# Kernel optimization log

Hardware: AMD Instinct MI355X
Metric: run time of the kernel (lower is better)

The kernel has to match this reference:

```python
import jax, jax.numpy as jnp
import numpy as np
import math

N_NODES = 100000
N_EDGES = 3200000
F_IN = 512
HID = 128
N_CLS = 16


def setup_inputs() -> dict:
    key = jax.random.key(0)
    k = jax.random.split(key, 6)
    x = jax.random.normal(k[0], (N_NODES, F_IN), dtype=jnp.float32)
    edge_index = jax.random.randint(k[1], (2, N_EDGES), 0, N_NODES, dtype=jnp.int32)
    W1 = jax.random.normal(k[2], (F_IN, HID), dtype=jnp.float32) / np.sqrt(F_IN)
    W2 = jax.random.normal(k[3], (HID, HID), dtype=jnp.float32) / np.sqrt(HID)
    W3 = jax.random.normal(k[4], (N_CLS, HID), dtype=jnp.float32) / np.sqrt(HID)
    b3 = jnp.zeros((N_CLS,), dtype=jnp.float32)
    return {"x": x, "edge_index": edge_index, "W1": W1, "W2": W2, "W3": W3, "b3": b3}


def _sym_norm(edge_index, num_nodes, dtype):
    # add self loops with fill_value = trunc(log2(average_node_degree))
    E = edge_index.shape[1]
    fill = float(math.trunc(math.log2(E / num_nodes)))
    loops = jnp.arange(num_nodes, dtype=edge_index.dtype)
    row = jnp.concatenate([edge_index[0], loops])
    col = jnp.concatenate([edge_index[1], loops])
    w = jnp.concatenate([jnp.ones((E,), dtype), jnp.full((num_nodes,), fill, dtype)])
    deg = jax.ops.segment_sum(w, row, num_segments=num_nodes)
    deg_inv_sqrt = jnp.where(deg > 0, jax.lax.rsqrt(deg), 0.0)
    norm = deg_inv_sqrt[row] * w * deg_inv_sqrt[col]
    return row, col, norm


def reference(x, edge_index, W1, W2, W3, b3):
    N = x.shape[0]
    row, col, norm = _sym_norm(edge_index, N, x.dtype)

    def gcn(h, W):
        h = h @ W                                   # [N, d_out]
        msg = norm[:, None] * h[col]                # gather + scale, [E', d_out]
        return jax.ops.segment_sum(msg, row, num_segments=N)

    h = jax.nn.relu(gcn(x, W1))      # layer 1 + srelu (threshold clamped at 0)
    h = gcn(h, W2)                   # layer 2
    # dropout p=0.5 is identity in eval mode
    return h @ W3.T + b3             # linear classifier [N, n_classes]
```

## Files before the change

kernel.cpp:

```cpp
#include <hip/hip_runtime.h>
#include <cmath>

typedef __attribute__((ext_vector_type(8))) short short8;
typedef __attribute__((ext_vector_type(8))) unsigned short ushort8;
typedef __attribute__((ext_vector_type(4))) float f32x4;
typedef __attribute__((ext_vector_type(2))) float f32x2;
typedef __attribute__((ext_vector_type(4))) unsigned int uint4v;
typedef __attribute__((ext_vector_type(2))) int int2v;

#define EPB 4096
#define BCAP 20480

__device__ inline float bf16_lo(unsigned int p) {
  union { unsigned int i; float f; } v; v.i = p << 16; return v.f;
}
__device__ inline float bf16_hi(unsigned int p) {
  union { unsigned int i; float f; } v; v.i = p & 0xffff0000u; return v.f;
}
__device__ inline f32x2 bf2(unsigned int p) {
  union { unsigned int i; float f; } lo, hi;
  lo.i = p << 16;
  hi.i = p & 0xffff0000u;
  return (f32x2){lo.f, hi.f};
}
__device__ inline float bf16u(unsigned short w) {
  union { unsigned int i; float f; } v; v.i = (unsigned int)w << 16; return v.f;
}
__device__ inline unsigned short f32_to_bf16(float f) {
  union { float f; unsigned int i; } v; v.f = f;
  unsigned int x = v.i;
  x += 0x7fffu + ((x >> 16) & 1u);
  return (unsigned short)(x >> 16);
}
__device__ inline unsigned int cvt_pk_bf16(float a, float b) {
  unsigned int r;
  asm("v_cvt_pk_bf16_f32 %0, %1, %2" : "=v"(r) : "v"(a), "v"(b));
  return r;
}
__device__ inline f32x2 pk_add(f32x2 a, f32x2 b) {
  f32x2 d;
  asm("v_pk_add_f32 %0, %1, %2" : "=v"(d) : "v"(a), "v"(b));
  return d;
}

__global__ __launch_bounds__(256) void bin_k(const int* __restrict__ rows,
                                             const int* __restrict__ cols,
                                             int* __restrict__ bucket_cursor,
                                             unsigned int* __restrict__ binned, int E) {
  __shared__ int lhist[256];
  __shared__ int gbase[256];
  __shared__ int loff[256];
  const int t = threadIdx.x;
  const int base = blockIdx.x * EPB;
  lhist[t] = 0;
  __syncthreads();

  int bk[16];
  unsigned int pk[16];
#pragma unroll
  for (int j = 0; j < 16; ++j) {
    int e = base + j * 256 + t;
    if (e < E) {
      int r = rows[e];
      int c = cols[e];
      bk[j] = r >> 9;
      pk[j] = ((unsigned int)(r & 511) << 17) | (unsigned int)c;
      atomicAdd(&lhist[bk[j]], 1);
    } else {
      bk[j] = -1;
    }
  }
  __syncthreads();
  if (lhist[t] > 0) gbase[t] = atomicAdd(&bucket_cursor[t], lhist[t]);
  loff[t] = 0;
  __syncthreads();
#pragma unroll
  for (int j = 0; j < 16; ++j) {
    if (bk[j] >= 0) {
      int rank = gbase[bk[j]] + atomicAdd(&loff[bk[j]], 1);
      if (rank < BCAP) binned[(size_t)bk[j] * BCAP + rank] = pk[j];
    }
  }
}

__global__ __launch_bounds__(1024) void bucket_csr_k(const unsigned int* __restrict__ binned,
                                                     const int* __restrict__ bucket_cursor,
                                                     int2v* __restrict__ rowse,
                                                     float* __restrict__ dis,
                                                     int* __restrict__ col_sorted,
                                                     int* __restrict__ perm,
                                                     int N, float fill) {
  __shared__ int lcnt[512];
  __shared__ int dh[512];
  __shared__ int wsum[16];
  const int b = blockIdx.x;
  const int t = threadIdx.x;
  const int start = b * BCAP;
  int cnt = bucket_cursor[b];
  if (cnt > BCAP) cnt = BCAP;
  const int endb = start + cnt;
  const int rbase = b << 9;

  auto scan512 = [&](int v) -> int {
    int x = v;
#pragma unroll
    for (int d = 1; d < 64; d <<= 1) {
      int u = __shfl_up(x, d, 64);
      if ((t & 63) >= d) x += u;
    }
    if (t < 512 && (t & 63) == 63) wsum[t >> 6] = x;
    __syncthreads();
    if (t < 64) {
      int s = (t < 8) ? wsum[t] : 0;
#pragma unroll
      for (int d = 1; d < 8; d <<= 1) {
        int u = __shfl_up(s, d, 64);
        if (t >= d) s += u;
      }
      if (t < 8) wsum[t] = s;
    }
    __syncthreads();
    int off = (t >= 64 && t < 512) ? wsum[(t >> 6) - 1] : 0;
    return x + off;
  };

  if (t < 512) lcnt[t] = 0;
  __syncthreads();
  for (int i = start + t; i < endb; i += 1024)
    atomicAdd(&lcnt[binned[i] >> 17], 1);
  __syncthreads();

  int v = (t < 512) ? lcnt[t] : 0;
  int incl = scan512(v);
  if (t < 512) {
    int excl = incl - v;
    int r = rbase + t;
    if (r < N) {
      rowse[r] = (int2v){start + excl, start + excl + v};
      float d = (float)v + fill;
      dis[r] = d > 0.f ? rsqrtf(d) : 0.f;
    }
    lcnt[t] = excl;
  }
  __syncthreads();

  if (t < 512) dh[t] = 0;
  __syncthreads();
  int key = 0;
  if (t < 512) {
    key = 511 - (v < 511 ? v : 511);
    atomicAdd(&dh[key], 1);
  }
  __syncthreads();
  int hv = (t < 512) ? dh[t] : 0;
  int hincl = scan512(hv);
  if (t < 512) dh[t] = hincl - hv;
  __syncthreads();
  if (t < 512) {
    int rank = atomicAdd(&dh[key], 1);
    perm[(b << 9) + rank] = rbase + t;
  }
  __syncthreads();

  for (int i = start + t; i < endb; i += 1024) {
    unsigned int pk = binned[i];
    int rl = (int)(pk >> 17);
    int c = (int)(pk & 0x1FFFFu);
    int pos = atomicAdd(&lcnt[rl], 1);
    col_sorted[start + pos] = c;
  }
}

__global__ __launch_bounds__(256) void cast_w_k(const float* __restrict__ W1,
                                                const float* __restrict__ W2,
                                                const float* __restrict__ W3,
                                                unsigned short* __restrict__ W1t,
                                                unsigned short* __restrict__ W2t,
                                                unsigned short* __restrict__ W3b,
                                                int FIN) {
  int g = blockIdx.x * 256 + threadIdx.x;
  int n1 = FIN * 128;
  if (g < n1) {
    int n = g & 127, k = g >> 7;
    W1t[n * FIN + k] = f32_to_bf16(W1[(size_t)k * 128 + n]);
  } else if (g < n1 + 128 * 128) {
    int gg = g - n1;
    int n = gg & 127, k = gg >> 7;
    W2t[n * 128 + k] = f32_to_bf16(W2[k * 128 + n]);
  } else if (g < n1 + 128 * 128 + 16 * 128) {
    int gg = g - n1 - 128 * 128;
    W3b[gg] = f32_to_bf16(W3[gg]);
  }
}

__global__ __launch_bounds__(256) void gemm_k(const void* __restrict__ Aq, int a_is_f32,
                                              int M, int K,
                                              const unsigned short* __restrict__ Bt,
                                              const float* __restrict__ dis,
                                              unsigned short* __restrict__ C) {
  __shared__ unsigned short Al[128 * 40];
  __shared__ unsigned short Bl[128 * 40];
  const int t = threadIdx.x;
  const int bm = blockIdx.x * 128;
  const int lane = t & 63;
  const int wave = t >> 6;
  const int wm = (wave >> 1) * 64;
  const int wn = (wave & 1) * 64;
  const int l15 = lane & 15;
  const int l4 = lane >> 4;

  f32x4 acc[4][4];
#pragma unroll
  for (int a = 0; a < 4; ++a)
#pragma unroll
    for (int b = 0; b < 4; ++b) acc[a][b] = (f32x4){0.f, 0.f, 0.f, 0.f};

  const int am = t >> 1;
  const int ak = (t & 1) * 16;
  const int bn = t >> 1;
  const int bk = (t & 1) * 16;
  const int arow = bm + am;
  const bool arow_ok = arow < M;

  auto load_a = [&](int k0, ushort8& o0, ushort8& o1) {
    o0 = (ushort8){0, 0, 0, 0, 0, 0, 0, 0};
    o1 = (ushort8){0, 0, 0, 0, 0, 0, 0, 0};
    if (arow_ok) {
      if (a_is_f32) {
        const float* p = (const float*)Aq + (size_t)arow * K + k0 + ak;
        f32x4 f0 = *(const f32x4*)(p);
        f32x4 f1 = *(const f32x4*)(p + 4);
        f32x4 f2 = *(const f32x4*)(p + 8);
        f32x4 f3 = *(const f32x4*)(p + 12);
        union { unsigned int u[4]; ushort8 v8; } c0, c1;
        c0.u[0] = cvt_pk_bf16(f0[0], f0[1]);
        c0.u[1] = cvt_pk_bf16(f0[2], f0[3]);
        c0.u[2] = cvt_pk_bf16(f1[0], f1[1]);
        c0.u[3] = cvt_pk_bf16(f1[2], f1[3]);
        c1.u[0] = cvt_pk_bf16(f2[0], f2[1]);
        c1.u[1] = cvt_pk_bf16(f2[2], f2[3]);
        c1.u[2] = cvt_pk_bf16(f3[0], f3[1]);
        c1.u[3] = cvt_pk_bf16(f3[2], f3[3]);
        o0 = c0.v8;
        o1 = c1.v8;
      } else {
        const unsigned short* p = (const unsigned short*)Aq + (size_t)arow * K + k0 + ak;
        o0 = *(const ushort8*)p;
        o1 = *(const ushort8*)(p + 8);
      }
    }
  };

  ushort8 av0, av1;
  load_a(0, av0, av1);
  ushort8 bv0 = *(const ushort8*)(Bt + (size_t)bn * K + bk);
  ushort8 bv1 = *(const ushort8*)(Bt + (size_t)bn * K + bk + 8);

  for (int k0 = 0; k0 < K; k0 += 32) {
    *(ushort8*)&Al[am * 40 + ak] = av0;
    *(ushort8*)&Al[am * 40 + ak + 8] = av1;
    *(ushort8*)&Bl[bn * 40 + bk] = bv0;
    *(ushort8*)&Bl[bn * 40 + bk + 8] = bv1;
    __syncthreads();

    const int kn = k0 + 32;
    if (kn < K) {
      load_a(kn, av0, av1);
      bv0 = *(const ushort8*)(Bt + (size_t)bn * K + kn + bk);
      bv1 = *(const ushort8*)(Bt + (size_t)bn * K + kn + bk + 8);
    }

    short8 af[4];
#pragma unroll
    for (int mt = 0; mt < 4; ++mt)
      af[mt] = *(const short8*)&Al[(wm + mt * 16 + l15) * 40 + l4 * 8];
#pragma unroll
    for (int nt = 0; nt < 4; ++nt) {
      short8 bfr = *(const short8*)&Bl[(wn + nt * 16 + l15) * 40 + l4 * 8];
#pragma unroll
      for (int mt = 0; mt < 4; ++mt)
        acc[mt][nt] = __builtin_amdgcn_mfma_f32_16x16x32_bf16(af[mt], bfr, acc[mt][nt], 0, 0, 0);
    }
    __syncthreads();
  }

#pragma unroll
  for (int mt = 0; mt < 4; ++mt) {
    int rbase = bm + wm + mt * 16 + l4 * 4;
#pragma unroll
    for (int r = 0; r < 4; ++r) {
      int row = rbase + r;
      if (row < M) {
        float dr = dis[row];
#pragma unroll
        for (int nt = 0; nt < 4; ++nt) {
          int col = wn + nt * 16 + l15;
          C[(size_t)row * 128 + col] = f32_to_bf16(acc[mt][nt][r] * dr);
        }
      }
    }
  }
}

__global__ __launch_bounds__(256) void agg_k(const unsigned short* __restrict__ hs,
                                             const int2v* __restrict__ rowse,
                                             const int* __restrict__ cols,
                                             const float* __restrict__ dis,
                                             const int* __restrict__ perm,
                                             unsigned short* __restrict__ out_bf,
                                             const unsigned short* __restrict__ W3b,
                                             const float* __restrict__ b3,
                                             float* __restrict__ fcout,
                                             int N, float fill, int mode) {
  const int q = blockIdx.x * 16 + (threadIdx.x >> 4);
  const unsigned int fl = threadIdx.x & 15;
  const int rid = __builtin_nontemporal_load(&perm[q]);
  if (rid >= N) return;
  const char* __restrict__ hsc = (const char*)hs;
  const unsigned int flo = fl << 4;

  int2v se = __builtin_nontemporal_load(&rowse[rid]);
  int e = se.x;
  const int end = se.y;

  f32x2 a0 = {0.f, 0.f}, a1 = {0.f, 0.f}, a2 = {0.f, 0.f}, a3 = {0.f, 0.f};

  for (; e + 8 <= end; e += 8) {
    unsigned int c0 = (unsigned int)__builtin_nontemporal_load(&cols[e]);
    unsigned int c1 = (unsigned int)__builtin_nontemporal_load(&cols[e + 1]);
    unsigned int c2 = (unsigned int)__builtin_nontemporal_load(&cols[e + 2]);
    unsigned int c3 = (unsigned int)__builtin_nontemporal_load(&cols[e + 3]);
    unsigned int c4 = (unsigned int)__builtin_nontemporal_load(&cols[e + 4]);
    unsigned int c5 = (unsigned int)__builtin_nontemporal_load(&cols[e + 5]);
    unsigned int c6 = (unsigned int)__builtin_nontemporal_load(&cols[e + 6]);
    unsigned int c7 = (unsigned int)__builtin_nontemporal_load(&cols[e + 7]);
    uint4v p0 = *(const uint4v*)(hsc + ((c0 << 8) | flo));
    uint4v p1 = *(const uint4v*)(hsc + ((c1 << 8) | flo));
    uint4v p2 = *(const uint4v*)(hsc + ((c2 << 8) | flo));
    uint4v p3 = *(const uint4v*)(hsc + ((c3 << 8) | flo));
    uint4v p4 = *(const uint4v*)(hsc + ((c4 << 8) | flo));
    uint4v p5 = *(const uint4v*)(hsc + ((c5 << 8) | flo));
    uint4v p6 = *(const uint4v*)(hsc + ((c6 << 8) | flo));
    uint4v p7 = *(const uint4v*)(hsc + ((c7 << 8) | flo));
    a0 = pk_add(a0, bf2(p0[0])); a1 = pk_add(a1, bf2(p0[1]));
    a2 = pk_add(a2, bf2(p0[2])); a3 = pk_add(a3, bf2(p0[3]));
    a0 = pk_add(a0, bf2(p1[0])); a1 = pk_add(a1, bf2(p1[1]));
    a2 = pk_add(a2, bf2(p1[2])); a3 = pk_add(a3, bf2(p1[3]));
    a0 = pk_add(a0, bf2(p2[0])); a1 = pk_add(a1, bf2(p2[1]));
    a2 = pk_add(a2, bf2(p2[2])); a3 = pk_add(a3, bf2(p2[3]));
    a0 = pk_add(a0, bf2(p3[0])); a1 = pk_add(a1, bf2(p3[1]));
    a2 = pk_add(a2, bf2(p3[2])); a3 = pk_add(a3, bf2(p3[3]));
    a0 = pk_add(a0, bf2(p4[0])); a1 = pk_add(a1, bf2(p4[1]));
    a2 = pk_add(a2, bf2(p4[2])); a3 = pk_add(a3, bf2(p4[3]));
    a0 = pk_add(a0, bf2(p5[0])); a1 = pk_add(a1, bf2(p5[1]));
    a2 = pk_add(a2, bf2(p5[2])); a3 = pk_add(a3, bf2(p5[3]));
    a0 = pk_add(a0, bf2(p6[0])); a1 = pk_add(a1, bf2(p6[1]));
    a2 = pk_add(a2, bf2(p6[2])); a3 = pk_add(a3, bf2(p6[3]));
    a0 = pk_add(a0, bf2(p7[0])); a1 = pk_add(a1, bf2(p7[1]));
    a2 = pk_add(a2, bf2(p7[2])); a3 = pk_add(a3, bf2(p7[3]));
  }
  for (; e + 4 <= end; e += 4) {
    unsigned int c0 = (unsigned int)__builtin_nontemporal_load(&cols[e]);
    unsigned int c1 = (unsigned int)__builtin_nontemporal_load(&cols[e + 1]);
    unsigned int c2 = (unsigned int)__builtin_nontemporal_load(&cols[e + 2]);
    unsigned int c3 = (unsigned int)__builtin_nontemporal_load(&cols[e + 3]);
    uint4v p0 = *(const uint4v*)(hsc + ((c0 << 8) | flo));
    uint4v p1 = *(const uint4v*)(hsc + ((c1 << 8) | flo));
    uint4v p2 = *(const uint4v*)(hsc + ((c2 << 8) | flo));
    uint4v p3 = *(const uint4v*)(hsc + ((c3 << 8) | flo));
    a0 = pk_add(a0, bf2(p0[0])); a1 = pk_add(a1, bf2(p0[1]));
    a2 = pk_add(a2, bf2(p0[2])); a3 = pk_add(a3, bf2(p0[3]));
    a0 = pk_add(a0, bf2(p1[0])); a1 = pk_add(a1, bf2(p1[1]));
    a2 = pk_add(a2, bf2(p1[2])); a3 = pk_add(a3, bf2(p1[3]));
    a0 = pk_add(a0, bf2(p2[0])); a1 = pk_add(a1, bf2(p2[1]));
    a2 = pk_add(a2, bf2(p2[2])); a3 = pk_add(a3, bf2(p2[3]));
    a0 = pk_add(a0, bf2(p3[0])); a1 = pk_add(a1, bf2(p3[1]));
    a2 = pk_add(a2, bf2(p3[2])); a3 = pk_add(a3, bf2(p3[3]));
  }
  for (; e < end; ++e) {
    unsigned int c = (unsigned int)__builtin_nontemporal_load(&cols[e]);
    uint4v p = *(const uint4v*)(hsc + ((c << 8) | flo));
    a0 = pk_add(a0, bf2(p[0])); a1 = pk_add(a1, bf2(p[1]));
    a2 = pk_add(a2, bf2(p[2])); a3 = pk_add(a3, bf2(p[3]));
  }

  uint4v ps = *(const uint4v*)(hsc + (((unsigned int)rid << 8) | flo));
  float dr = dis[rid];
  float v[8];
  v[0] = dr * (a0.x + fill * bf16_lo(ps[0]));
  v[1] = dr * (a0.y + fill * bf16_hi(ps[0]));
  v[2] = dr * (a1.x + fill * bf16_lo(ps[1]));
  v[3] = dr * (a1.y + fill * bf16_hi(ps[1]));
  v[4] = dr * (a2.x + fill * bf16_lo(ps[2]));
  v[5] = dr * (a2.y + fill * bf16_hi(ps[2]));
  v[6] = dr * (a3.x + fill * bf16_lo(ps[3]));
  v[7] = dr * (a3.y + fill * bf16_hi(ps[3]));

  if (mode == 0) {
    uint4v o;
#pragma unroll
    for (int k = 0; k < 4; ++k) {
      float f0 = fmaxf(v[2 * k], 0.f);
      float f1 = fmaxf(v[2 * k + 1], 0.f);
      o[k] = cvt_pk_bf16(f0, f1);
    }
    __builtin_nontemporal_store(o, (uint4v*)((char*)out_bf + (((unsigned int)rid << 8) | flo)));
  } else {
    float p[16];
#pragma unroll
    for (int c = 0; c < 16; ++c) {
      ushort8 wr = *(const ushort8*)(W3b + c * 128 + fl * 8);
      float s = v[0] * bf16u(wr[0]);
      s = fmaf(v[1], bf16u(wr[1]), s);
      s = fmaf(v[2], bf16u(wr[2]), s);
      s = fmaf(v[3], bf16u(wr[3]), s);
      s = fmaf(v[4], bf16u(wr[4]), s);
      s = fmaf(v[5], bf16u(wr[5]), s);
      s = fmaf(v[6], bf16u(wr[6]), s);
      s = fmaf(v[7], bf16u(wr[7]), s);
      p[c] = s;
    }
#pragma unroll
    for (int m = 1; m <= 8; m <<= 1)
#pragma unroll
      for (int c = 0; c < 16; ++c) p[c] += __shfl_xor(p[c], m);
    fcout[(size_t)rid * 16 + fl] = p[fl] + b3[fl];
  }
}

extern "C" void kernel_launch(void* const* d_in, const int* in_sizes, int n_in,
                              void* d_out, int out_size, void* d_ws, size_t ws_size,
                              hipStream_t stream) {
  const float* x  = (const float*)d_in[0];
  const int* edge = (const int*)d_in[1];
  const float* W1 = (const float*)d_in[2];
  const float* W2 = (const float*)d_in[3];
  const float* W3 = (const float*)d_in[4];
  const float* b3 = (const float*)d_in[5];
  float* out = (float*)d_out;

  const int HID = 128;
  const int FIN = in_sizes[2] / HID;
  const int N   = in_sizes[0] / FIN;
  const int E   = in_sizes[1] / 2;
  const float fill = truncf(log2f((float)E / (float)N));

  char* w = (char*)d_ws;
  size_t off = 0;
  auto alloc = [&](size_t bytes) -> void* {
    void* p = w + off;
    off += (bytes + 255) & ~(size_t)255;
    return p;
  };
  const int NB = (N + 511) >> 9;
  float* dis      = (float*)alloc((size_t)N * 4);
  int2v* rowse    = (int2v*)alloc((size_t)N * 8);
  int* perm       = (int*)alloc((size_t)NB * 512 * 4);
  int* col_sorted = (int*)alloc((size_t)NB * BCAP * 4);
  int* bucket_cursor = (int*)alloc(256 * 4);
  unsigned int* binned = (unsigned int*)alloc((size_t)NB * BCAP * 4);
  unsigned short* W1t  = (unsigned short*)alloc((size_t)FIN * 128 * 2);
  unsigned short* W2t  = (unsigned short*)alloc(128 * 128 * 2);
  unsigned short* W3b  = (unsigned short*)alloc(16 * 128 * 2);
  unsigned short* bufA = (unsigned short*)alloc((size_t)N * 128 * 2);
  unsigned short* bufB = (unsigned short*)alloc((size_t)N * 128 * 2);

  const int* rows  = edge;
  const int* colsp = edge + E;

  hipMemsetAsync(bucket_cursor, 0, 256 * 4, stream);
  bin_k<<<(E + EPB - 1) / EPB, 256, 0, stream>>>(rows, colsp, bucket_cursor, binned, E);
  bucket_csr_k<<<NB, 1024, 0, stream>>>(binned, bucket_cursor, rowse, dis,
                                        col_sorted, perm, N, fill);
  const int castN = FIN * 128 + 128 * 128 + 16 * 128;
  cast_w_k<<<(castN + 255) / 256, 256, 0, stream>>>(W1, W2, W3, W1t, W2t, W3b, FIN);

  const int gm = (N + 127) / 128;
  gemm_k<<<gm, 256, 0, stream>>>(x, 1, N, FIN, W1t, dis, bufA);
  agg_k<<<NB * 32, 256, 0, stream>>>(bufA, rowse, col_sorted, dis, perm, bufB,
                                     W3b, b3, out, N, fill, 0);
  gemm_k<<<gm, 256, 0, stream>>>(bufB, 0, N, HID, W2t, dis, bufA);
  agg_k<<<NB * 32, 256, 0, stream>>>(bufA, rowse, col_sorted, dis, perm, bufB,
                                     W3b, b3, out, N, fill, 1);
}
```

Baseline: 670.7 us.

## Replace bucket binning CSR build with global degree count, scan, and atomic scatter

Replaces the two-pass bucket binning (shared-memory histogram, then per-bucket local sort) with a global per-row atomic degree count, a per-block scan that sets row offsets and cursors, and a global atomic scatter of columns into CSR slots. This drops the intermediate binned buffer and its read/write traffic, but adds 3.2M global atomics on row counters twice, and column order within a row becomes nondeterministic. The aggregation kernel also switches its nontemporal loads and stores to ordinary cached ones.

Result: slower. 983.8 us (+46.7%).

```diff
diff --git a/kernel.cpp b/kernel.cpp
--- a/kernel.cpp
+++ b/kernel.cpp
@@ -7,8 +7,8 @@
 typedef __attribute__((ext_vector_type(2))) float f32x2;
 typedef __attribute__((ext_vector_type(4))) unsigned int uint4v;
 typedef __attribute__((ext_vector_type(2))) int int2v;
-
-#define EPB 4096
+typedef __attribute__((ext_vector_type(4))) int int4v;
+
 #define BCAP 20480
 
 __device__ inline float bf16_lo(unsigned int p) {
@@ -43,131 +43,115 @@
   return d;
 }
 
-__global__ __launch_bounds__(256) void bin_k(const int* __restrict__ rows,
-                                             const int* __restrict__ cols,
-                                             int* __restrict__ bucket_cursor,
-                                             unsigned int* __restrict__ binned, int E) {
-  __shared__ int lhist[256];
-  __shared__ int gbase[256];
-  __shared__ int loff[256];
-  const int t = threadIdx.x;
-  const int base = blockIdx.x * EPB;
-  lhist[t] = 0;
-  __syncthreads();
-
-  int bk[16];
-  unsigned int pk[16];
-#pragma unroll
-  for (int j = 0; j < 16; ++j) {
-    int e = base + j * 256 + t;
-    if (e < E) {
-      int r = rows[e];
-      int c = cols[e];
-      bk[j] = r >> 9;
-      pk[j] = ((unsigned int)(r & 511) << 17) | (unsigned int)c;
-      atomicAdd(&lhist[bk[j]], 1);
-    } else {
-      bk[j] = -1;
-    }
-  }
-  __syncthreads();
-  if (lhist[t] > 0) gbase[t] = atomicAdd(&bucket_cursor[t], lhist[t]);
-  loff[t] = 0;
-  __syncthreads();
-#pragma unroll
-  for (int j = 0; j < 16; ++j) {
-    if (bk[j] >= 0) {
-      int rank = gbase[bk[j]] + atomicAdd(&loff[bk[j]], 1);
-      if (rank < BCAP) binned[(size_t)bk[j] * BCAP + rank] = pk[j];
-    }
-  }
-}
-
-__global__ __launch_bounds__(1024) void bucket_csr_k(const unsigned int* __restrict__ binned,
-                                                     const int* __restrict__ bucket_cursor,
-                                                     int2v* __restrict__ rowse,
-                                                     float* __restrict__ dis,
-                                                     int* __restrict__ col_sorted,
-                                                     int* __restrict__ perm,
-                                                     int N, float fill) {
-  __shared__ int lcnt[512];
+__global__ __launch_bounds__(256) void deg_k(const int* __restrict__ rows,
+                                             int* __restrict__ deg, int E) {
+  int i = (blockIdx.x * 256 + threadIdx.x) * 4;
+  if (i + 4 <= E) {
+    int4v r4 = *(const int4v*)(rows + i);
+    atomicAdd(&deg[r4[0]], 1);
+    atomicAdd(&deg[r4[1]], 1);
+    atomicAdd(&deg[r4[2]], 1);
+    atomicAdd(&deg[r4[3]], 1);
+  } else {
+    for (int e = i; e < E; ++e) atomicAdd(&deg[rows[e]], 1);
+  }
+}
+
+__global__ __launch_bounds__(512) void scan_k(const int* __restrict__ deg,
+                                              int2v* __restrict__ rowse,
+                                              float* __restrict__ dis,
+                                              int* __restrict__ cursor,
+                                              int* __restrict__ perm,
+                                              int N, float fill) {
+  __shared__ int wsum[8];
   __shared__ int dh[512];
-  __shared__ int wsum[16];
   const int b = blockIdx.x;
   const int t = threadIdx.x;
+  const int rbase = b << 9;
   const int start = b * BCAP;
-  int cnt = bucket_cursor[b];
-  if (cnt > BCAP) cnt = BCAP;
-  const int endb = start + cnt;
-  const int rbase = b << 9;
-
-  auto scan512 = [&](int v) -> int {
-    int x = v;
-#pragma unroll
-    for (int d = 1; d < 64; d <<= 1) {
-      int u = __shfl_up(x, d, 64);
-      if ((t & 63) >= d) x += u;
-    }
-    if (t < 512 && (t & 63) == 63) wsum[t >> 6] = x;
-    __syncthreads();
-    if (t < 64) {
-      int s = (t < 8) ? wsum[t] : 0;
-#pragma unroll
-      for (int d = 1; d < 8; d <<= 1) {
-        int u = __shfl_up(s, d, 64);
-        if (t >= d) s += u;
-      }
-      if (t < 8) wsum[t] = s;
-    }
-    __syncthreads();
-    int off = (t >= 64 && t < 512) ? wsum[(t >> 6) - 1] : 0;
-    return x + off;
-  };
-
-  if (t < 512) lcnt[t] = 0;
-  __syncthreads();
-  for (int i = start + t; i < endb; i += 1024)
-    atomicAdd(&lcnt[binned[i] >> 17], 1);
-  __syncthreads();
-
-  int v = (t < 512) ? lcnt[t] : 0;
-  int incl = scan512(v);
-  if (t < 512) {
-    int excl = incl - v;
-    int r = rbase + t;
-    if (r < N) {
-      rowse[r] = (int2v){start + excl, start + excl + v};
-      float d = (float)v + fill;
-      dis[r] = d > 0.f ? rsqrtf(d) : 0.f;
-    }
-    lcnt[t] = excl;
-  }
-  __syncthreads();
-
-  if (t < 512) dh[t] = 0;
-  __syncthreads();
-  int key = 0;
-  if (t < 512) {
-    key = 511 - (v < 511 ? v : 511);
-    atomicAdd(&dh[key], 1);
-  }
-  __syncthreads();
-  int hv = (t < 512) ? dh[t] : 0;
-  int hincl = scan512(hv);
-  if (t < 512) dh[t] = hincl - hv;
-  __syncthreads();
-  if (t < 512) {
-    int rank = atomicAdd(&dh[key], 1);
-    perm[(b << 9) + rank] = rbase + t;
-  }
-  __syncthreads();
-
-  for (int i = start + t; i < endb; i += 1024) {
-    unsigned int pk = binned[i];
-    int rl = (int)(pk >> 17);
-    int c = (int)(pk & 0x1FFFFu);
-    int pos = atomicAdd(&lcnt[rl], 1);
-    col_sorted[start + pos] = c;
+
+  int v = deg[rbase + t];
+
+  int x = v;
+#pragma unroll
+  for (int d = 1; d < 64; d <<= 1) {
+    int u = __shfl_up(x, d, 64);
+    if ((t & 63) >= d) x += u;
+  }
+  if ((t & 63) == 63) wsum[t >> 6] = x;
+  __syncthreads();
+  if (t < 64) {
+    int s = (t < 8) ? wsum[t] : 0;
+#pragma unroll
+    for (int d = 1; d < 8; d <<= 1) {
+      int u = __shfl_up(s, d, 64);
+      if (t >= d) s += u;
+    }
+    if (t < 8) wsum[t] = s;
+  }
+  __syncthreads();
+  int incl = x + ((t >= 64) ? wsum[(t >> 6) - 1] : 0);
+  int excl = incl - v;
+
+  const int r = rbase + t;
+  if (r < N) {
+    rowse[r] = (int2v){start + excl, start + excl + v};
+    float d = (float)v + fill;
+    dis[r] = d > 0.f ? rsqrtf(d) : 0.f;
+  }
+  cursor[r] = start + excl;
+
+  dh[t] = 0;
+  __syncthreads();
+  int key = 511 - (v < 511 ? v : 511);
+  atomicAdd(&dh[key], 1);
+  __syncthreads();
+  int hv = dh[t];
+  int hx = hv;
+#pragma unroll
+  for (int d = 1; d < 64; d <<= 1) {
+    int u = __shfl_up(hx, d, 64);
+    if ((t & 63) >= d) hx += u;
+  }
+  if ((t & 63) == 63) wsum[t >> 6] = hx;
+  __syncthreads();
+  if (t < 64) {
+    int s = (t < 8) ? wsum[t] : 0;
+#pragma unroll
+    for (int d = 1; d < 8; d <<= 1) {
+      int u = __shfl_up(s, d, 64);
+      if (t >= d) s += u;
+    }
+    if (t < 8) wsum[t] = s;
+  }
+  __syncthreads();
+  int hincl = hx + ((t >= 64) ? wsum[(t >> 6) - 1] : 0);
+  dh[t] = hincl - hv;
+  __syncthreads();
+  int rank = atomicAdd(&dh[key], 1);
+  perm[rbase + rank] = r;
+}
+
+__global__ __launch_bounds__(256) void scat_k(const int* __restrict__ rows,
+                                              const int* __restrict__ cols,
+                                              int* __restrict__ cursor,
+                                              int* __restrict__ col_sorted, int E) {
+  int i = (blockIdx.x * 256 + threadIdx.x) * 4;
+  if (i + 4 <= E) {
+    int4v r4 = *(const int4v*)(rows + i);
+    int4v c4 = *(const int4v*)(cols + i);
+#pragma unroll
+    for (int j = 0; j < 4; ++j) {
+      int r = r4[j];
+      int pos = atomicAdd(&cursor[r], 1);
+      if (pos < (r >> 9) * BCAP + BCAP) col_sorted[pos] = c4[j];
+    }
+  } else {
+    for (int e = i; e < E; ++e) {
+      int r = rows[e];
+      int pos = atomicAdd(&cursor[r], 1);
+      if (pos < (r >> 9) * BCAP + BCAP) col_sorted[pos] = cols[e];
+    }
   }
 }
 
@@ -314,26 +298,26 @@
                                              int N, float fill, int mode) {
   const int q = blockIdx.x * 16 + (threadIdx.x >> 4);
   const unsigned int fl = threadIdx.x & 15;
-  const int rid = __builtin_nontemporal_load(&perm[q]);
+  const int rid = perm[q];
   if (rid >= N) return;
   const char* __restrict__ hsc = (const char*)hs;
   const unsigned int flo = fl << 4;
 
-  int2v se = __builtin_nontemporal_load(&rowse[rid]);
+  int2v se = rowse[rid];
   int e = se.x;
   const int end = se.y;
 
   f32x2 a0 = {0.f, 0.f}, a1 = {0.f, 0.f}, a2 = {0.f, 0.f}, a3 = {0.f, 0.f};
 
   for (; e + 8 <= end; e += 8) {
-    unsigned int c0 = (unsigned int)__builtin_nontemporal_load(&cols[e]);
-    unsigned int c1 = (unsigned int)__builtin_nontemporal_load(&cols[e + 1]);
-    unsigned int c2 = (unsigned int)__builtin_nontemporal_load(&cols[e + 2]);
-    unsigned int c3 = (unsigned int)__builtin_nontemporal_load(&cols[e + 3]);
-    unsigned int c4 = (unsigned int)__builtin_nontemporal_load(&cols[e + 4]);
-    unsigned int c5 = (unsigned int)__builtin_nontemporal_load(&cols[e + 5]);
-    unsigned int c6 = (unsigned int)__builtin_nontemporal_load(&cols[e + 6]);
-    unsigned int c7 = (unsigned int)__builtin_nontemporal_load(&cols[e + 7]);
+    unsigned int c0 = (unsigned int)cols[e];
+    unsigned int c1 = (unsigned int)cols[e + 1];
+    unsigned int c2 = (unsigned int)cols[e + 2];
+    unsigned int c3 = (unsigned int)cols[e + 3];
+    unsigned int c4 = (unsigned int)cols[e + 4];
+    unsigned int c5 = (unsigned int)cols[e + 5];
+    unsigned int c6 = (unsigned int)cols[e + 6];
+    unsigned int c7 = (unsigned int)cols[e + 7];
     uint4v p0 = *(const uint4v*)(hsc + ((c0 << 8) | flo));
     uint4v p1 = *(const uint4v*)(hsc + ((c1 << 8) | flo));
     uint4v p2 = *(const uint4v*)(hsc + ((c2 << 8) | flo));
@@ -360,10 +344,10 @@
     a2 = pk_add(a2, bf2(p7[2])); a3 = pk_add(a3, bf2(p7[3]));
   }
   for (; e + 4 <= end; e += 4) {
-    unsigned int c0 = (unsigned int)__builtin_nontemporal_load(&cols[e]);
-    unsigned int c1 = (unsigned int)__builtin_nontemporal_load(&cols[e + 1]);
-    unsigned int c2 = (unsigned int)__builtin_nontemporal_load(&cols[e + 2]);
-    unsigned int c3 = (unsigned int)__builtin_nontemporal_load(&cols[e + 3]);
+    unsigned int c0 = (unsigned int)cols[e];
+    unsigned int c1 = (unsigned int)cols[e + 1];
+    unsigned int c2 = (unsigned int)cols[e + 2];
+    unsigned int c3 = (unsigned int)cols[e + 3];
     uint4v p0 = *(const uint4v*)(hsc + ((c0 << 8) | flo));
     uint4v p1 = *(const uint4v*)(hsc + ((c1 << 8) | flo));
     uint4v p2 = *(const uint4v*)(hsc + ((c2 << 8) | flo));
@@ -378,7 +362,7 @@
     a2 = pk_add(a2, bf2(p3[2])); a3 = pk_add(a3, bf2(p3[3]));
   }
   for (; e < end; ++e) {
-    unsigned int c = (unsigned int)__builtin_nontemporal_load(&cols[e]);
+    unsigned int c = (unsigned int)cols[e];
     uint4v p = *(const uint4v*)(hsc + ((c << 8) | flo));
     a0 = pk_add(a0, bf2(p[0])); a1 = pk_add(a1, bf2(p[1]));
     a2 = pk_add(a2, bf2(p[2])); a3 = pk_add(a3, bf2(p[3]));
@@ -404,7 +388,7 @@
       float f1 = fmaxf(v[2 * k + 1], 0.f);
       o[k] = cvt_pk_bf16(f0, f1);
     }
-    __builtin_nontemporal_store(o, (uint4v*)((char*)out_bf + (((unsigned int)rid << 8) | flo)));
+    *(uint4v*)((char*)out_bf + (((unsigned int)rid << 8) | flo)) = o;
   } else {
     float p[16];
 #pragma unroll
@@ -453,12 +437,13 @@
     return p;
   };
   const int NB = (N + 511) >> 9;
+  const int NR = NB * 512;
   float* dis      = (float*)alloc((size_t)N * 4);
   int2v* rowse    = (int2v*)alloc((size_t)N * 8);
-  int* perm       = (int*)alloc((size_t)NB * 512 * 4);
+  int* perm       = (int*)alloc((size_t)NR * 4);
   int* col_sorted = (int*)alloc((size_t)NB * BCAP * 4);
-  int* bucket_cursor = (int*)alloc(256 * 4);
-  unsigned int* binned = (unsigned int*)alloc((size_t)NB * BCAP * 4);
+  int* deg        = (int*)alloc((size_t)NR * 4);
+  int* cursor     = (int*)alloc((size_t)NR * 4);
   unsigned short* W1t  = (unsigned short*)alloc((size_t)FIN * 128 * 2);
   unsigned short* W2t  = (unsigned short*)alloc(128 * 128 * 2);
   unsigned short* W3b  = (unsigned short*)alloc(16 * 128 * 2);
@@ -468,10 +453,11 @@
   const int* rows  = edge;
   const int* colsp = edge + E;
 
-  hipMemsetAsync(bucket_cursor, 0, 256 * 4, stream);
-  bin_k<<<(E + EPB - 1) / EPB, 256, 0, stream>>>(rows, colsp, bucket_cursor, binned, E);
-  bucket_csr_k<<<NB, 1024, 0, stream>>>(binned, bucket_cursor, rowse, dis,
-                                        col_sorted, perm, N, fill);
+  hipMemsetAsync(deg, 0, (size_t)NR * 4, stream);
+  const int eg = ((E + 3) / 4 + 255) / 256;
+  deg_k<<<eg, 256, 0, stream>>>(rows, deg, E);
+  scan_k<<<NB, 512, 0, stream>>>(deg, rowse, dis, cursor, perm, N, fill);
+  scat_k<<<eg, 256, 0, stream>>>(rows, colsp, cursor, col_sorted, E);
   const int castN = FIN * 128 + 128 * 128 + 16 * 128;
   cast_w_k<<<(castN + 255) / 256, 256, 0, stream>>>(W1, W2, W3, W1t, W2t, W3b, FIN);
 
```

## Sort bucket entries in LDS and drop nontemporal hints in aggregation

Applied to the files above, without the earlier changes.

The per-bucket CSR kernel now loads each bucket's binned entries once into registers, counts and scatters them into an LDS array, then writes col_sorted coalesced. The old version read binned from global memory twice and scattered directly to global. Separately, the aggregation kernel replaces nontemporal loads and stores with ordinary ones so the cols, rowse and perm streams and the output can use the cache normally. The LDS buffer of 20480 ints (80KB) limits occupancy of the sort kernel to about one block per CU.

After: 639.4 us. 4.7% less time.

```diff
diff --git a/kernel.cpp b/kernel.cpp
--- a/kernel.cpp
+++ b/kernel.cpp
@@ -83,23 +83,24 @@
   }
 }
 
-__global__ __launch_bounds__(1024) void bucket_csr_k(const unsigned int* __restrict__ binned,
-                                                     const int* __restrict__ bucket_cursor,
-                                                     int2v* __restrict__ rowse,
-                                                     float* __restrict__ dis,
-                                                     int* __restrict__ col_sorted,
-                                                     int* __restrict__ perm,
-                                                     int N, float fill) {
-  __shared__ int lcnt[512];
+__global__ __launch_bounds__(1024) void sort_k(const unsigned int* __restrict__ binned,
+                                               const int* __restrict__ bucket_cursor,
+                                               int2v* __restrict__ rowse,
+                                               float* __restrict__ dis,
+                                               int* __restrict__ col_sorted,
+                                               int* __restrict__ perm,
+                                               int N, float fill) {
+  __shared__ int sorted[BCAP];
+  __shared__ int cnt[512];
+  __shared__ int cur[512];
   __shared__ int dh[512];
-  __shared__ int wsum[16];
+  __shared__ int wsum[8];
   const int b = blockIdx.x;
   const int t = threadIdx.x;
   const int start = b * BCAP;
-  int cnt = bucket_cursor[b];
-  if (cnt > BCAP) cnt = BCAP;
-  const int endb = start + cnt;
   const int rbase = b << 9;
+  int c = bucket_cursor[b];
+  if (c > BCAP) c = BCAP;
 
   auto scan512 = [&](int v) -> int {
     int x = v;
@@ -124,25 +125,46 @@
     return x + off;
   };
 
-  if (t < 512) lcnt[t] = 0;
-  __syncthreads();
-  for (int i = start + t; i < endb; i += 1024)
-    atomicAdd(&lcnt[binned[i] >> 17], 1);
-  __syncthreads();
-
-  int v = (t < 512) ? lcnt[t] : 0;
+  unsigned int ent[20];
+#pragma unroll
+  for (int j = 0; j < 20; ++j) {
+    int i = j * 1024 + t;
+    ent[j] = (i < c) ? binned[start + i] : 0xFFFFFFFFu;
+  }
+
+  if (t < 512) cnt[t] = 0;
+  __syncthreads();
+#pragma unroll
+  for (int j = 0; j < 20; ++j)
+    if (ent[j] != 0xFFFFFFFFu) atomicAdd(&cnt[ent[j] >> 17], 1);
+  __syncthreads();
+
+  int v = (t < 512) ? cnt[t] : 0;
   int incl = scan512(v);
+  int excl = incl - v;
   if (t < 512) {
-    int excl = incl - v;
+    cur[t] = excl;
     int r = rbase + t;
     if (r < N) {
       rowse[r] = (int2v){start + excl, start + excl + v};
       float d = (float)v + fill;
       dis[r] = d > 0.f ? rsqrtf(d) : 0.f;
     }
-    lcnt[t] = excl;
-  }
-  __syncthreads();
+  }
+  __syncthreads();
+
+#pragma unroll
+  for (int j = 0; j < 20; ++j) {
+    if (ent[j] != 0xFFFFFFFFu) {
+      int rl = (int)(ent[j] >> 17);
+      int pos = atomicAdd(&cur[rl], 1);
+      sorted[pos] = (int)(ent[j] & 0x1FFFFu);
+    }
+  }
+  __syncthreads();
+
+  for (int i = t; i < c; i += 1024)
+    col_sorted[start + i] = sorted[i];
 
   if (t < 512) dh[t] = 0;
   __syncthreads();
@@ -158,16 +180,7 @@
   __syncthreads();
   if (t < 512) {
     int rank = atomicAdd(&dh[key], 1);
-    perm[(b << 9) + rank] = rbase + t;
-  }
-  __syncthreads();
-
-  for (int i = start + t; i < endb; i += 1024) {
-    unsigned int pk = binned[i];
-    int rl = (int)(pk >> 17);
-    int c = (int)(pk & 0x1FFFFu);
-    int pos = atomicAdd(&lcnt[rl], 1);
-    col_sorted[start + pos] = c;
+    perm[rbase + rank] = rbase + t;
   }
 }
 
@@ -314,26 +327,26 @@
                                              int N, float fill, int mode) {
   const int q = blockIdx.x * 16 + (threadIdx.x >> 4);
   const unsigned int fl = threadIdx.x & 15;
-  const int rid = __builtin_nontemporal_load(&perm[q]);
+  const int rid = perm[q];
   if (rid >= N) return;
   const char* __restrict__ hsc = (const char*)hs;
   const unsigned int flo = fl << 4;
 
-  int2v se = __builtin_nontemporal_load(&rowse[rid]);
+  int2v se = rowse[rid];
   int e = se.x;
   const int end = se.y;
 
   f32x2 a0 = {0.f, 0.f}, a1 = {0.f, 0.f}, a2 = {0.f, 0.f}, a3 = {0.f, 0.f};
 
   for (; e + 8 <= end; e += 8) {
-    unsigned int c0 = (unsigned int)__builtin_nontemporal_load(&cols[e]);
-    unsigned int c1 = (unsigned int)__builtin_nontemporal_load(&cols[e + 1]);
-    unsigned int c2 = (unsigned int)__builtin_nontemporal_load(&cols[e + 2]);
-    unsigned int c3 = (unsigned int)__builtin_nontemporal_load(&cols[e + 3]);
-    unsigned int c4 = (unsigned int)__builtin_nontemporal_load(&cols[e + 4]);
-    unsigned int c5 = (unsigned int)__builtin_nontemporal_load(&cols[e + 5]);
-    unsigned int c6 = (unsigned int)__builtin_nontemporal_load(&cols[e + 6]);
-    unsigned int c7 = (unsigned int)__builtin_nontemporal_load(&cols[e + 7]);
+    unsigned int c0 = (unsigned int)cols[e];
+    unsigned int c1 = (unsigned int)cols[e + 1];
+    unsigned int c2 = (unsigned int)cols[e + 2];
+    unsigned int c3 = (unsigned int)cols[e + 3];
+    unsigned int c4 = (unsigned int)cols[e + 4];
+    unsigned int c5 = (unsigned int)cols[e + 5];
+    unsigned int c6 = (unsigned int)cols[e + 6];
+    unsigned int c7 = (unsigned int)cols[e + 7];
     uint4v p0 = *(const uint4v*)(hsc + ((c0 << 8) | flo));
     uint4v p1 = *(const uint4v*)(hsc + ((c1 << 8) | flo));
     uint4v p2 = *(const uint4v*)(hsc + ((c2 << 8) | flo));
@@ -360,10 +373,10 @@
     a2 = pk_add(a2, bf2(p7[2])); a3 = pk_add(a3, bf2(p7[3]));
   }
   for (; e + 4 <= end; e += 4) {
-    unsigned int c0 = (unsigned int)__builtin_nontemporal_load(&cols[e]);
-    unsigned int c1 = (unsigned int)__builtin_nontemporal_load(&cols[e + 1]);
-    unsigned int c2 = (unsigned int)__builtin_nontemporal_load(&cols[e + 2]);
-    unsigned int c3 = (unsigned int)__builtin_nontemporal_load(&cols[e + 3]);
+    unsigned int c0 = (unsigned int)cols[e];
+    unsigned int c1 = (unsigned int)cols[e + 1];
+    unsigned int c2 = (unsigned int)cols[e + 2];
+    unsigned int c3 = (unsigned int)cols[e + 3];
     uint4v p0 = *(const uint4v*)(hsc + ((c0 << 8) | flo));
     uint4v p1 = *(const uint4v*)(hsc + ((c1 << 8) | flo));
     uint4v p2 = *(const uint4v*)(hsc + ((c2 << 8) | flo));
@@ -378,7 +391,7 @@
     a2 = pk_add(a2, bf2(p3[2])); a3 = pk_add(a3, bf2(p3[3]));
   }
   for (; e < end; ++e) {
-    unsigned int c = (unsigned int)__builtin_nontemporal_load(&cols[e]);
+    unsigned int c = (unsigned int)cols[e];
     uint4v p = *(const uint4v*)(hsc + ((c << 8) | flo));
     a0 = pk_add(a0, bf2(p[0])); a1 = pk_add(a1, bf2(p[1]));
     a2 = pk_add(a2, bf2(p[2])); a3 = pk_add(a3, bf2(p[3]));
@@ -404,7 +417,7 @@
       float f1 = fmaxf(v[2 * k + 1], 0.f);
       o[k] = cvt_pk_bf16(f0, f1);
     }
-    __builtin_nontemporal_store(o, (uint4v*)((char*)out_bf + (((unsigned int)rid << 8) | flo)));
+    *(uint4v*)((char*)out_bf + (((unsigned int)rid << 8) | flo)) = o;
   } else {
     float p[16];
 #pragma unroll
@@ -470,8 +483,8 @@
 
   hipMemsetAsync(bucket_cursor, 0, 256 * 4, stream);
   bin_k<<<(E + EPB - 1) / EPB, 256, 0, stream>>>(rows, colsp, bucket_cursor, binned, E);
-  bucket_csr_k<<<NB, 1024, 0, stream>>>(binned, bucket_cursor, rowse, dis,
-                                        col_sorted, perm, N, fill);
+  sort_k<<<NB, 1024, 0, stream>>>(binned, bucket_cursor, rowse, dis,
+                                  col_sorted, perm, N, fill);
   const int castN = FIN * 128 + 128 * 128 + 16 * 128;
   cast_w_k<<<(castN + 255) / 256, 256, 0, stream>>>(W1, W2, W3, W1t, W2t, W3b, FIN);
 
```
